# Kernel optimization log

Hardware: AMD Instinct MI355X
Metric: run time of the kernel (lower is better)

Reference implementation:

```python
import jax, jax.numpy as jnp
import numpy as np

B, S, D, H = 4, 2048, 512, 8
HD = D // H  # head_dim = 64


def setup_inputs() -> dict:
    key = jax.random.key(0)
    ks = jax.random.split(key, 6)
    s = 1.0 / np.sqrt(D)
    return {
        "value": jax.random.normal(ks[0], (B, S, D), jnp.float32),
        "key": jax.random.normal(ks[1], (B, S, D), jnp.float32),
        "query": jax.random.normal(ks[2], (B, S, D), jnp.float32),
        "Wv": jax.random.normal(ks[3], (D, D), jnp.float32) * s,
        "bv": jnp.zeros((D,), jnp.float32),
        "Wk": jax.random.normal(ks[4], (D, D), jnp.float32) * s,
        "bk": jnp.zeros((D,), jnp.float32),
        "Wq": jax.random.normal(ks[5], (D, D), jnp.float32) * s,
        "bq": jnp.zeros((D,), jnp.float32),
    }


def _heads(x):
    # [B,S,D] -> [B,H,S,hd]
    return x.reshape(B, S, H, HD).transpose(0, 2, 1, 3)


def reference(value, key, query, Wv, bv, Wk, bk, Wq, bq):
    v = _heads(value @ Wv.T + bv)
    k = _heads(key @ Wk.T + bk)
    q = _heads(query @ Wq.T + bq)
    scale = 1.0 / jnp.sqrt(jnp.asarray(HD, q.dtype))
    # two scaled-dot-product score maps, each [B,H,S,S]
    att_kq = jax.nn.softmax(jnp.einsum("bhqd,bhkd->bhqk", q, k) * scale, axis=-1)
    att_vq = jax.nn.softmax(jnp.einsum("bhqd,bhkd->bhqk", q, v) * scale, axis=-1)
    att_map = att_kq + att_vq
    fused = v + k  # [B,H,S,hd]
    attended = jnp.einsum("bhqk,bhkd->bhqd", att_map, fused)
    # elementwise multiply with q, reduce over the sequence (query) axis
    head_logits = jnp.sum(attended * q, axis=2)  # [B,H,hd]
    return head_logits.reshape(B, H * HD)
```

## Files before the change

### kernel.cpp

```cpp
#include <hip/hip_runtime.h>
#include <hip/hip_bf16.h>

#define Bq 4
#define Sq 2048
#define Dq 512
#define Hq 8
#define HDq 64

typedef __attribute__((ext_vector_type(8))) short short8;
typedef __attribute__((ext_vector_type(4))) float f32x4;

#if __has_builtin(__builtin_amdgcn_exp2f)
#define EXP2(x) __builtin_amdgcn_exp2f(x)
#else
#define EXP2(x) exp2f(x)
#endif

#define SCALE2 (0.125f * 1.44269504088896340736f)
#define INV_SCALE2 (5.545177444479562f)

__device__ __forceinline__ short bfs(float x) {
    __hip_bfloat16 h = __float2bfloat16(x);
    short r;
    __builtin_memcpy(&r, &h, 2);
    return r;
}

__device__ __forceinline__ short8 cvt8(float4 a, float4 b) {
    union { __hip_bfloat16 h[8]; short8 s; } u;
    u.h[0] = __float2bfloat16(a.x); u.h[1] = __float2bfloat16(a.y);
    u.h[2] = __float2bfloat16(a.z); u.h[3] = __float2bfloat16(a.w);
    u.h[4] = __float2bfloat16(b.x); u.h[5] = __float2bfloat16(b.y);
    u.h[6] = __float2bfloat16(b.z); u.h[7] = __float2bfloat16(b.w);
    return u.s;
}

__device__ __forceinline__ void gload16(const void* g, void* l) {
    __builtin_amdgcn_global_load_lds(
        (const __attribute__((address_space(1))) unsigned int*)g,
        (__attribute__((address_space(3))) unsigned int*)l, 16, 0, 0);
}

__global__ __launch_bounds__(256, 3)
void proj_kernel(const float* __restrict__ Xv, const float* __restrict__ Xk, const float* __restrict__ Xq,
                 const float* __restrict__ Wv, const float* __restrict__ Wk, const float* __restrict__ Wq,
                 const float* __restrict__ bv, const float* __restrict__ bk, const float* __restrict__ bq,
                 __hip_bfloat16* __restrict__ Ov, __hip_bfloat16* __restrict__ Ok, __hip_bfloat16* __restrict__ Oq) {
    __shared__ alignas(16) short As[128 * 64];
    __shared__ alignas(16) short Bs[128 * 64];

    const int z = blockIdx.z;
    const float* X   = (z == 0) ? Xv : (z == 1) ? Xk : Xq;
    const float* W   = (z == 0) ? Wv : (z == 1) ? Wk : Wq;
    const float* bia = (z == 0) ? bv : (z == 1) ? bk : bq;
    __hip_bfloat16* O = (z == 0) ? Ov : (z == 1) ? Ok : Oq;
    const float sc = (z == 2) ? SCALE2 : 1.0f;

    const int tid  = threadIdx.x;
    const int lane = tid & 63;
    const int w    = tid >> 6;
    const int wr   = w >> 1;
    const int wc   = w & 1;
    const int m0   = blockIdx.y * 128;
    const int n0   = blockIdx.x * 128;
    const int arow = lane & 15;
    const int ag   = lane >> 4;

    f32x4 acc[4][4];
    #pragma unroll
    for (int t = 0; t < 4; ++t)
        #pragma unroll
        for (int u = 0; u < 4; ++u) acc[t][u] = (f32x4){0.f, 0.f, 0.f, 0.f};

    for (int kk = 0; kk < Dq / 64; ++kk) {
        __syncthreads();
        #pragma unroll
        for (int p = 0; p < 4; ++p) {
            int id  = p * 256 + tid;
            int row = id >> 3;
            int c   = id & 7;
            int dst = row * 128 + ((c * 16) ^ ((row & 7) << 4));
            const float* ax = X + (size_t)(m0 + row) * Dq + kk * 64 + c * 8;
            const float* bx = W + (size_t)(n0 + row) * Dq + kk * 64 + c * 8;
            float4 a0 = *(const float4*)ax;
            float4 a1 = *(const float4*)(ax + 4);
            float4 b0 = *(const float4*)bx;
            float4 b1 = *(const float4*)(bx + 4);
            *(short8*)((char*)As + dst) = cvt8(a0, a1);
            *(short8*)((char*)Bs + dst) = cvt8(b0, b1);
        }
        __syncthreads();
        #pragma unroll
        for (int h = 0; h < 2; ++h) {
            short8 af[4], bf[4];
            #pragma unroll
            for (int t = 0; t < 4; ++t) {
                int ra = wr * 64 + t * 16 + arow;
                int rb = wc * 64 + t * 16 + arow;
                af[t] = *(const short8*)((const char*)As + ra * 128 + ((h * 64 + ag * 16) ^ ((ra & 7) << 4)));
                bf[t] = *(const short8*)((const char*)Bs + rb * 128 + ((h * 64 + ag * 16) ^ ((rb & 7) << 4)));
            }
            #pragma unroll
            for (int t = 0; t < 4; ++t)
                #pragma unroll
                for (int u = 0; u < 4; ++u)
                    acc[t][u] = __builtin_amdgcn_mfma_f32_16x16x32_bf16(af[t], bf[u], acc[t][u], 0, 0, 0);
        }
    }

    float biasv[4];
    #pragma unroll
    for (int u = 0; u < 4; ++u) biasv[u] = bia[n0 + wc * 64 + u * 16 + arow];

    #pragma unroll
    for (int t = 0; t < 4; ++t) {
        #pragma unroll
        for (int u = 0; u < 4; ++u) {
            #pragma unroll
            for (int r = 0; r < 4; ++r) {
                int m = m0 + wr * 64 + t * 16 + 4 * ag + r;
                int n = n0 + wc * 64 + u * 16 + arow;
                int b = m >> 11, s = m & 2047;
                int hh = n >> 6, hd = n & 63;
                O[((((size_t)b * Hq + hh) * Sq + s) << 6) + hd] =
                    __float2bfloat16((acc[t][u][r] + biasv[u]) * sc);
            }
        }
    }
}

__global__ __launch_bounds__(256)
void fuse_t_kernel(const __hip_bfloat16* __restrict__ Kh, const __hip_bfloat16* __restrict__ Vh,
                   __hip_bfloat16* __restrict__ Ft) {
    __shared__ float T[64][65];
    const int bh = blockIdx.x >> 5;
    const int st = blockIdx.x & 31;
    const int tid = threadIdx.x;

    #pragma unroll
    for (int p = 0; p < 2; ++p) {
        int idx = p * 256 + tid;
        int r = idx >> 3;
        int c = (idx & 7) * 8;
        size_t g = ((size_t)bh * Sq + st * 64 + r) * 64 + c;
        float4 k4 = *(const float4*)((const char*)Kh + g * 2);
        float4 v4 = *(const float4*)((const char*)Vh + g * 2);
        const __hip_bfloat16* kp = (const __hip_bfloat16*)&k4;
        const __hip_bfloat16* vp = (const __hip_bfloat16*)&v4;
        #pragma unroll
        for (int j = 0; j < 8; ++j)
            T[r][c + j] = __bfloat162float(kp[j]) + __bfloat162float(vp[j]);
    }
    __syncthreads();
    #pragma unroll
    for (int pp = 0; pp < 2; ++pp) {
        int idx = pp * 256 + tid;
        int d  = idx >> 3;
        int p8 = (idx & 7) * 8;
        alignas(16) __hip_bfloat16 tmp[8];
        #pragma unroll
        for (int j2 = 0; j2 < 8; ++j2) {
            int p = p8 + j2;
            int h  = p >> 5;
            int ag = (p >> 3) & 3;
            int j  = p & 7;
            int k  = 16 * (2 * (j >> 2) + h) + 4 * ag + (j & 3);
            tmp[j2] = __float2bfloat16(T[k][d]);
        }
        *(float4*)((char*)Ft + (((size_t)bh * 64 + d) * Sq + st * 64 + p8) * 2) = *(const float4*)tmp;
    }
}

__global__ __launch_bounds__(256, 2)
void attn_kernel(const __hip_bfloat16* __restrict__ Qh, const __hip_bfloat16* __restrict__ Kh,
                 const __hip_bfloat16* __restrict__ Vh, const __hip_bfloat16* __restrict__ Ft,
                 float* __restrict__ part) {
    __shared__ alignas(16) short Qs[128 * 64];
    __shared__ alignas(16) short Ks[64 * 64];
    __shared__ alignas(16) short Vs[64 * 64];
    __shared__ alignas(16) short Fs[64 * 64];

    const int tid  = threadIdx.x;
    const int lane = tid & 63;
    const int w    = tid >> 6;
    const int lb   = (blockIdx.x & 7) * 64 + (blockIdx.x >> 3);
    const int bh   = lb >> 4;
    const int s0   = (lb & 15) * 128;

    const char* Qbh = (const char*)(Qh + (size_t)bh * Sq * 64);
    const char* Kbh = (const char*)(Kh + (size_t)bh * Sq * 64);
    const char* Vbh = (const char*)(Vh + (size_t)bh * Sq * 64);
    const char* Fbh = (const char*)(Ft + (size_t)bh * 64 * Sq);

    #pragma unroll
    for (int p = 0; p < 4; ++p) {
        int idx = p * 256 + tid;
        int r = idx >> 3;
        int c = idx & 7;
        int swz = (r & 7) << 4;
        float4 q4 = *(const float4*)(Qbh + ((size_t)(s0 + r) * 64 + c * 8) * 2);
        *(float4*)((char*)Qs + r * 128 + ((c * 16) ^ swz)) = q4;
    }
    __syncthreads();

    const int arow = lane & 15;
    const int ag   = lane >> 4;

    short8 qa[2][2];
    #pragma unroll
    for (int tile = 0; tile < 2; ++tile) {
        int qr = w * 32 + tile * 16 + arow;
        int qswz = (qr & 7) << 4;
        qa[tile][0] = *(const short8*)((const char*)Qs + qr * 128 + ((16 * ag) ^ qswz));
        qa[tile][1] = *(const short8*)((const char*)Qs + qr * 128 + ((64 + 16 * ag) ^ qswz));
    }

    short8 ones;
    #pragma unroll
    for (int j = 0; j < 8; ++j) ones[j] = (short)0x3F80;

    f32x4 acc_k[2][4], acc_v[2][4];
    f32x4 acc_lk[2], acc_lv[2];
    #pragma unroll
    for (int tile = 0; tile < 2; ++tile) {
        #pragma unroll
        for (int t = 0; t < 4; ++t) {
            acc_k[tile][t] = (f32x4){0.f, 0.f, 0.f, 0.f};
            acc_v[tile][t] = (f32x4){0.f, 0.f, 0.f, 0.f};
        }
        acc_lk[tile] = (f32x4){0.f, 0.f, 0.f, 0.f};
        acc_lv[tile] = (f32x4){0.f, 0.f, 0.f, 0.f};
    }

    int srow[2], sbyte[2];
    size_t kof[2], fof[2];
    #pragma unroll
    for (int p = 0; p < 2; ++p) {
        srow[p] = p * 32 + w * 8 + (lane >> 3);
        int scs = (lane & 7) ^ (srow[p] & 7);
        sbyte[p] = p * 4096 + w * 1024;
        kof[p] = ((size_t)srow[p] * 64 + scs * 8) * 2;
        fof[p] = ((size_t)srow[p] * Sq + scs * 8) * 2;
    }

    for (int ck = 0; ck < Sq / 64; ++ck) {
        const size_t kv0 = (size_t)ck * 64;
        __syncthreads();
        #pragma unroll
        for (int p = 0; p < 2; ++p) {
            gload16(Kbh + kv0 * 128 + kof[p], (char*)Ks + sbyte[p]);
            gload16(Vbh + kv0 * 128 + kof[p], (char*)Vs + sbyte[p]);
            gload16(Fbh + fof[p] + kv0 * 2,   (char*)Fs + sbyte[p]);
        }
        __syncthreads();

        f32x4 sk[2][4], sv[2][4];
        #pragma unroll
        for (int tile = 0; tile < 2; ++tile)
            #pragma unroll
            for (int t = 0; t < 4; ++t) {
                sk[tile][t] = (f32x4){0.f, 0.f, 0.f, 0.f};
                sv[tile][t] = (f32x4){0.f, 0.f, 0.f, 0.f};
            }
        __builtin_amdgcn_s_setprio(1);
        #pragma unroll
        for (int t = 0; t < 4; ++t) {
            int brow = t * 16 + arow;
            int bswz = (brow & 7) << 4;
            short8 kb0 = *(const short8*)((const char*)Ks + brow * 128 + ((16 * ag) ^ bswz));
            short8 kb1 = *(const short8*)((const char*)Ks + brow * 128 + ((64 + 16 * ag) ^ bswz));
            short8 vb0 = *(const short8*)((const char*)Vs + brow * 128 + ((16 * ag) ^ bswz));
            short8 vb1 = *(const short8*)((const char*)Vs + brow * 128 + ((64 + 16 * ag) ^ bswz));
            #pragma unroll
            for (int tile = 0; tile < 2; ++tile) {
                sk[tile][t] = __builtin_amdgcn_mfma_f32_16x16x32_bf16(kb0, qa[tile][0], sk[tile][t], 0, 0, 0);
                sk[tile][t] = __builtin_amdgcn_mfma_f32_16x16x32_bf16(kb1, qa[tile][1], sk[tile][t], 0, 0, 0);
                sv[tile][t] = __builtin_amdgcn_mfma_f32_16x16x32_bf16(vb0, qa[tile][0], sv[tile][t], 0, 0, 0);
                sv[tile][t] = __builtin_amdgcn_mfma_f32_16x16x32_bf16(vb1, qa[tile][1], sv[tile][t], 0, 0, 0);
            }
        }
        __builtin_amdgcn_s_setprio(0);

        short8 bpk[2][2], bpv[2][2];
        #pragma unroll
        for (int tile = 0; tile < 2; ++tile) {
            #pragma unroll
            for (int t = 0; t < 4; ++t) {
                #pragma unroll
                for (int r = 0; r < 4; ++r) {
                    bpk[tile][t & 1][4 * (t >> 1) + r] = bfs(EXP2(sk[tile][t][r]));
                    bpv[tile][t & 1][4 * (t >> 1) + r] = bfs(EXP2(sv[tile][t][r]));
                }
            }
        }

        __builtin_amdgcn_s_setprio(1);
        #pragma unroll
        for (int td = 0; td < 4; ++td) {
            int row = td * 16 + arow;
            int rswz = (row & 7) << 4;
            short8 fa0 = *(const short8*)((const char*)Fs + row * 128 + ((16 * ag) ^ rswz));
            short8 fa1 = *(const short8*)((const char*)Fs + row * 128 + ((64 + 16 * ag) ^ rswz));
            #pragma unroll
            for (int tile = 0; tile < 2; ++tile) {
                acc_k[tile][td] = __builtin_amdgcn_mfma_f32_16x16x32_bf16(fa0, bpk[tile][0], acc_k[tile][td], 0, 0, 0);
                acc_k[tile][td] = __builtin_amdgcn_mfma_f32_16x16x32_bf16(fa1, bpk[tile][1], acc_k[tile][td], 0, 0, 0);
                acc_v[tile][td] = __builtin_amdgcn_mfma_f32_16x16x32_bf16(fa0, bpv[tile][0], acc_v[tile][td], 0, 0, 0);
                acc_v[tile][td] = __builtin_amdgcn_mfma_f32_16x16x32_bf16(fa1, bpv[tile][1], acc_v[tile][td], 0, 0, 0);
            }
        }
        #pragma unroll
        for (int tile = 0; tile < 2; ++tile) {
            acc_lk[tile] = __builtin_amdgcn_mfma_f32_16x16x32_bf16(ones, bpk[tile][0], acc_lk[tile], 0, 0, 0);
            acc_lk[tile] = __builtin_amdgcn_mfma_f32_16x16x32_bf16(ones, bpk[tile][1], acc_lk[tile], 0, 0, 0);
            acc_lv[tile] = __builtin_amdgcn_mfma_f32_16x16x32_bf16(ones, bpv[tile][0], acc_lv[tile], 0, 0, 0);
            acc_lv[tile] = __builtin_amdgcn_mfma_f32_16x16x32_bf16(ones, bpv[tile][1], acc_lv[tile], 0, 0, 0);
        }
        __builtin_amdgcn_s_setprio(0);
    }

    __syncthreads();
    float* part_s = (float*)Ks;
    #pragma unroll
    for (int tile = 0; tile < 2; ++tile) {
        float ilk = INV_SCALE2 / acc_lk[tile][0];
        float ilv = INV_SCALE2 / acc_lv[tile][0];

        int qr = w * 32 + tile * 16 + arow;
        f32x4 c[4];
        #pragma unroll
        for (int td = 0; td < 4; ++td) {
            #pragma unroll
            for (int r = 0; r < 4; ++r) {
                int d = 16 * td + 4 * ag + r;
                int byte = 2 * d;
                float qv = __bfloat162float(*(const __hip_bfloat16*)(
                    (const char*)Qs + qr * 128 + (((byte & ~15) ^ ((qr & 7) << 4)) | (byte & 15))));
                c[td][r] = (acc_k[tile][td][r] * ilk + acc_v[tile][td][r] * ilv) * qv;
            }
        }
        #pragma unroll
        for (int off = 1; off < 16; off <<= 1) {
            #pragma unroll
            for (int td = 0; td < 4; ++td) {
                #pragma unroll
                for (int r = 0; r < 4; ++r) c[td][r] += __shfl_xor(c[td][r], off);
            }
        }
        if (arow == 0) {
            #pragma unroll
            for (int td = 0; td < 4; ++td)
                #pragma unroll
                for (int r = 0; r < 4; ++r)
                    part_s[(w * 2 + tile) * 64 + 16 * td + 4 * ag + r] = c[td][r];
        }
    }
    __syncthreads();
    if (tid < 64) {
        float t = 0.f;
        #pragma unroll
        for (int r = 0; r < 8; ++r) t += part_s[r * 64 + tid];
        part[(size_t)lb * 64 + tid] = t;
    }
}

__global__ void reduce_kernel(const float* __restrict__ part, float* __restrict__ out) {
    int bh = blockIdx.x;
    int d  = threadIdx.x;
    float t = 0.f;
    for (int i = 0; i < 16; ++i)
        t += part[(size_t)(bh * 16 + i) * 64 + d];
    out[bh * 64 + d] = t;
}

extern "C" void kernel_launch(void* const* d_in, const int* in_sizes, int n_in,
                              void* d_out, int out_size, void* d_ws, size_t ws_size,
                              hipStream_t stream) {
    const float* value = (const float*)d_in[0];
    const float* key   = (const float*)d_in[1];
    const float* query = (const float*)d_in[2];
    const float* Wv    = (const float*)d_in[3];
    const float* bv    = (const float*)d_in[4];
    const float* Wk    = (const float*)d_in[5];
    const float* bk    = (const float*)d_in[6];
    const float* Wq    = (const float*)d_in[7];
    const float* bq    = (const float*)d_in[8];
    float* out = (float*)d_out;

    char* w = (char*)d_ws;
    __hip_bfloat16* Qh = (__hip_bfloat16*)(w);
    __hip_bfloat16* Kh = (__hip_bfloat16*)(w + (size_t)8  * 1024 * 1024);
    __hip_bfloat16* Vh = (__hip_bfloat16*)(w + (size_t)16 * 1024 * 1024);
    __hip_bfloat16* Ft = (__hip_bfloat16*)(w + (size_t)24 * 1024 * 1024);
    float*          part = (float*)      (w + (size_t)32 * 1024 * 1024);

    dim3 pg(Dq / 128, (Bq * Sq) / 128, 3);
    proj_kernel<<<pg, 256, 0, stream>>>(value, key, query, Wv, Wk, Wq, bv, bk, bq, Vh, Kh, Qh);

    fuse_t_kernel<<<1024, 256, 0, stream>>>(Kh, Vh, Ft);
    attn_kernel<<<512, 256, 0, stream>>>(Qh, Kh, Vh, Ft, part);
    reduce_kernel<<<32, 64, 0, stream>>>(part, out);
}
```

Measured before the change: 120.7 us.

## Fold K+V fused transposed tensor into projection kernel as fourth z-slice

Removes the separate fuse_t_kernel and instead has the projection kernel compute K+V directly as a concatenated-K GEMM ([Xk|Xv] times [Wk|Wv], 16 k-steps) in a fourth z-slice. The result gets the summed bias, is transposed through shared memory and is written in the permuted Ft layout. This drops one launch and the re-read of Kh/Vh, at the cost of redundant GEMM work (a double-length GEMM for the extra slice) and larger shared memory in every proj block, which may reduce occupancy. Ft is now summed in fp32 before bf16 rounding, which slightly changes numerics.

Result: slower. 130.1 us (+7.8%).

```diff
diff --git a/kernel.cpp b/kernel.cpp
--- a/kernel.cpp
+++ b/kernel.cpp
@@ -45,9 +45,11 @@
 void proj_kernel(const float* __restrict__ Xv, const float* __restrict__ Xk, const float* __restrict__ Xq,
                  const float* __restrict__ Wv, const float* __restrict__ Wk, const float* __restrict__ Wq,
                  const float* __restrict__ bv, const float* __restrict__ bk, const float* __restrict__ bq,
-                 __hip_bfloat16* __restrict__ Ov, __hip_bfloat16* __restrict__ Ok, __hip_bfloat16* __restrict__ Oq) {
-    __shared__ alignas(16) short As[128 * 64];
-    __shared__ alignas(16) short Bs[128 * 64];
+                 __hip_bfloat16* __restrict__ Ov, __hip_bfloat16* __restrict__ Ok, __hip_bfloat16* __restrict__ Oq,
+                 __hip_bfloat16* __restrict__ Ft) {
+    __shared__ alignas(16) short Smem[128 * 130];
+    short* AsP = Smem;
+    short* BsP = Smem + 128 * 64;
 
     const int z = blockIdx.z;
     const float* X   = (z == 0) ? Xv : (z == 1) ? Xk : Xq;
@@ -72,7 +74,18 @@
         #pragma unroll
         for (int u = 0; u < 4; ++u) acc[t][u] = (f32x4){0.f, 0.f, 0.f, 0.f};
 
-    for (int kk = 0; kk < Dq / 64; ++kk) {
+    const int kmax = (z == 3) ? 16 : 8;
+    for (int kk = 0; kk < kmax; ++kk) {
+        const float* Xe = X;
+        const float* We = W;
+        int kc;
+        if (z == 3) {
+            Xe = (kk < 8) ? Xk : Xv;
+            We = (kk < 8) ? Wk : Wv;
+            kc = (kk & 7) * 64;
+        } else {
+            kc = kk * 64;
+        }
         __syncthreads();
         #pragma unroll
         for (int p = 0; p < 4; ++p) {
@@ -80,14 +93,14 @@
             int row = id >> 3;
             int c   = id & 7;
             int dst = row * 128 + ((c * 16) ^ ((row & 7) << 4));
-            const float* ax = X + (size_t)(m0 + row) * Dq + kk * 64 + c * 8;
-            const float* bx = W + (size_t)(n0 + row) * Dq + kk * 64 + c * 8;
+            const float* ax = Xe + (size_t)(m0 + row) * Dq + kc + c * 8;
+            const float* bx = We + (size_t)(n0 + row) * Dq + kc + c * 8;
             float4 a0 = *(const float4*)ax;
             float4 a1 = *(const float4*)(ax + 4);
             float4 b0 = *(const float4*)bx;
             float4 b1 = *(const float4*)(bx + 4);
-            *(short8*)((char*)As + dst) = cvt8(a0, a1);
-            *(short8*)((char*)Bs + dst) = cvt8(b0, b1);
+            *(short8*)((char*)AsP + dst) = cvt8(a0, a1);
+            *(short8*)((char*)BsP + dst) = cvt8(b0, b1);
         }
         __syncthreads();
         #pragma unroll
@@ -97,8 +110,8 @@
             for (int t = 0; t < 4; ++t) {
                 int ra = wr * 64 + t * 16 + arow;
                 int rb = wc * 64 + t * 16 + arow;
-                af[t] = *(const short8*)((const char*)As + ra * 128 + ((h * 64 + ag * 16) ^ ((ra & 7) << 4)));
-                bf[t] = *(const short8*)((const char*)Bs + rb * 128 + ((h * 64 + ag * 16) ^ ((rb & 7) << 4)));
+                af[t] = *(const short8*)((const char*)AsP + ra * 128 + ((h * 64 + ag * 16) ^ ((ra & 7) << 4)));
+                bf[t] = *(const short8*)((const char*)BsP + rb * 128 + ((h * 64 + ag * 16) ^ ((rb & 7) << 4)));
             }
             #pragma unroll
             for (int t = 0; t < 4; ++t)
@@ -110,64 +123,64 @@
 
     float biasv[4];
     #pragma unroll
-    for (int u = 0; u < 4; ++u) biasv[u] = bia[n0 + wc * 64 + u * 16 + arow];
-
-    #pragma unroll
-    for (int t = 0; t < 4; ++t) {
-        #pragma unroll
-        for (int u = 0; u < 4; ++u) {
-            #pragma unroll
-            for (int r = 0; r < 4; ++r) {
-                int m = m0 + wr * 64 + t * 16 + 4 * ag + r;
-                int n = n0 + wc * 64 + u * 16 + arow;
-                int b = m >> 11, s = m & 2047;
-                int hh = n >> 6, hd = n & 63;
-                O[((((size_t)b * Hq + hh) * Sq + s) << 6) + hd] =
-                    __float2bfloat16((acc[t][u][r] + biasv[u]) * sc);
-            }
-        }
-    }
-}
-
-__global__ __launch_bounds__(256)
-void fuse_t_kernel(const __hip_bfloat16* __restrict__ Kh, const __hip_bfloat16* __restrict__ Vh,
-                   __hip_bfloat16* __restrict__ Ft) {
-    __shared__ float T[64][65];
-    const int bh = blockIdx.x >> 5;
-    const int st = blockIdx.x & 31;
-    const int tid = threadIdx.x;
-
-    #pragma unroll
-    for (int p = 0; p < 2; ++p) {
-        int idx = p * 256 + tid;
-        int r = idx >> 3;
-        int c = (idx & 7) * 8;
-        size_t g = ((size_t)bh * Sq + st * 64 + r) * 64 + c;
-        float4 k4 = *(const float4*)((const char*)Kh + g * 2);
-        float4 v4 = *(const float4*)((const char*)Vh + g * 2);
-        const __hip_bfloat16* kp = (const __hip_bfloat16*)&k4;
-        const __hip_bfloat16* vp = (const __hip_bfloat16*)&v4;
-        #pragma unroll
-        for (int j = 0; j < 8; ++j)
-            T[r][c + j] = __bfloat162float(kp[j]) + __bfloat162float(vp[j]);
-    }
-    __syncthreads();
-    #pragma unroll
-    for (int pp = 0; pp < 2; ++pp) {
-        int idx = pp * 256 + tid;
-        int d  = idx >> 3;
-        int p8 = (idx & 7) * 8;
-        alignas(16) __hip_bfloat16 tmp[8];
-        #pragma unroll
-        for (int j2 = 0; j2 < 8; ++j2) {
-            int p = p8 + j2;
-            int h  = p >> 5;
-            int ag = (p >> 3) & 3;
-            int j  = p & 7;
-            int k  = 16 * (2 * (j >> 2) + h) + 4 * ag + (j & 3);
-            tmp[j2] = __float2bfloat16(T[k][d]);
-        }
-        *(float4*)((char*)Ft + (((size_t)bh * 64 + d) * Sq + st * 64 + p8) * 2) = *(const float4*)tmp;
+    for (int u = 0; u < 4; ++u) {
+        int n = n0 + wc * 64 + u * 16 + arow;
+        biasv[u] = (z == 3) ? (bk[n] + bv[n]) : bia[n];
+    }
+
+    if (z < 3) {
+        #pragma unroll
+        for (int t = 0; t < 4; ++t) {
+            #pragma unroll
+            for (int u = 0; u < 4; ++u) {
+                #pragma unroll
+                for (int r = 0; r < 4; ++r) {
+                    int m = m0 + wr * 64 + t * 16 + 4 * ag + r;
+                    int n = n0 + wc * 64 + u * 16 + arow;
+                    int b = m >> 11, s = m & 2047;
+                    int hh = n >> 6, hd = n & 63;
+                    O[((((size_t)b * Hq + hh) * Sq + s) << 6) + hd] =
+                        __float2bfloat16((acc[t][u][r] + biasv[u]) * sc);
+                }
+            }
+        }
+    } else {
+        __syncthreads();
+        #pragma unroll
+        for (int t = 0; t < 4; ++t) {
+            #pragma unroll
+            for (int u = 0; u < 4; ++u) {
+                int nl = wc * 64 + u * 16 + arow;
+                #pragma unroll
+                for (int r = 0; r < 4; ++r) {
+                    int ml = wr * 64 + t * 16 + 4 * ag + r;
+                    Smem[nl * 130 + ml] = bfs(acc[t][u][r] + biasv[u]);
+                }
+            }
+        }
+        __syncthreads();
+        int nl = tid & 127;
+        int ch = tid >> 7;
+        int ng = n0 + nl;
+        int hh = ng >> 6, d = ng & 63;
+        int b  = m0 >> 11;
+        int sbase = (m0 & 2047) + ch * 64;
+        char* outp = (char*)Ft + (((size_t)(b * Hq + hh) * 64 + d) * Sq + sbase) * 2;
+        const short* trow = Smem + nl * 130 + ch * 64;
+        #pragma unroll
+        for (int g = 0; g < 8; ++g) {
+            alignas(16) short tmp[8];
+            #pragma unroll
+            for (int j2 = 0; j2 < 8; ++j2) {
+                int p  = g * 8 + j2;
+                int h2 = p >> 5;
+                int a2 = (p >> 3) & 3;
+                int j  = p & 7;
+                int k  = 16 * (2 * (j >> 2) + h2) + 4 * a2 + (j & 3);
+                tmp[j2] = trow[k];
+            }
+            *(float4*)(outp + g * 16) = *(const float4*)tmp;
+        }
     }
 }
 
@@ -394,10 +407,10 @@
     __hip_bfloat16* Ft = (__hip_bfloat16*)(w + (size_t)24 * 1024 * 1024);
     float*          part = (float*)      (w + (size_t)32 * 1024 * 1024);
 
-    dim3 pg(Dq / 128, (Bq * Sq) / 128, 3);
-    proj_kernel<<<pg, 256, 0, stream>>>(value, key, query, Wv, Wk, Wq, bv, bk, bq, Vh, Kh, Qh);
-
-    fuse_t_kernel<<<1024, 256, 0, stream>>>(Kh, Vh, Ft);
+    dim3 pg(Dq / 128, (Bq * Sq) / 128, 4);
+    proj_kernel<<<pg, 256, 0, stream>>>(value, key, query, Wv, Wk, Wq, bv, bk, bq,
+                                        Vh, Kh, Qh, Ft);
+
     attn_kernel<<<512, 256, 0, stream>>>(Qh, Kh, Vh, Ft, part);
     reduce_kernel<<<32, 64, 0, stream>>>(part, out);
 }
```
